# Kernel optimization log

Measured on AMD Instinct MI355X. Metric: run time of the kernel, lower is better.

The kernel has to match this reference:

```python
import jax, jax.numpy as jnp
import numpy as np

H = 4                 # num_heads
GATE_NORM = 16.0      # gate_logit_normalizer
EPS = 1e-5            # RMSNorm eps


def setup_inputs() -> dict:
    key = jax.random.key(0)
    ks = jax.random.split(key, 12)
    B, T, D = 8, 4096, 1024
    Dk_total, Dv_total, Dlow = D // 2, D, 16

    def w(k, shape, fan_in):
        return jax.random.normal(k, shape, dtype=jnp.float32) * (fan_in ** -0.5)

    return {
        "x": jax.random.normal(ks[0], (B, T, D), dtype=jnp.float32),
        "Wq": w(ks[1], (D, Dk_total), D),
        "Wk": w(ks[2], (D, Dk_total), D),
        "Wv": w(ks[3], (D, Dv_total), D),
        "gk_w1": w(ks[4], (D, Dlow), D),
        "gk_w2": w(ks[5], (Dlow, Dk_total), Dlow),
        "gk_b2": jnp.zeros((Dk_total,), dtype=jnp.float32),
        "Wg": w(ks[6], (D, Dv_total), D),
        "g_norm_w": jnp.ones((Dv_total // H,), dtype=jnp.float32),
        "Wo": w(ks[7], (Dv_total, D), Dv_total),
    }


def _gla_forward(x, Wq, Wk, Wv, gk_w1, gk_w2, gk_b2, Wg, g_norm_w, Wo):
    B, T, D = x.shape
    Dk = Wq.shape[1] // H
    Dv = Wv.shape[1] // H

    q = (x @ Wq).reshape(B, T, H, Dk) * (Dk ** -0.5)
    k = (x @ Wk).reshape(B, T, H, Dk)
    v = (x @ Wv).reshape(B, T, H, Dv)
    # low-rank gate logits -> log-space decay gk (<= 0)
    gk = jax.nn.log_sigmoid((x @ gk_w1) @ gk_w2 + gk_b2) / GATE_NORM
    gk = gk.reshape(B, T, H, Dk)

    # recurrent gated linear attention:
    #   S_t = exp(gk_t)[:, None] * S_{t-1} + k_t^T v_t ;  o_t = q_t @ S_t
    def step(S, qkvg):
        qt, kt, vt, gt = qkvg          # each [B, H, Dk|Dv]
        S = jnp.exp(gt)[..., None] * S + kt[..., None] * vt[..., None, :]
        ot = jnp.einsum("bhk,bhkv->bhv", qt, S)
        return S, ot

    S0 = jnp.zeros((B, H, Dk, Dv), dtype=x.dtype)
    tm = lambda a: jnp.swapaxes(a, 0, 1)  # [B,T,...] -> [T,B,...]
    _, o = jax.lax.scan(step, S0, (tm(q), tm(k), tm(v), tm(gk)))
    o = jnp.swapaxes(o, 0, 1)            # [B, T, H, Dv]

    # output gate: RMSNorm(o) * swish(g), per head
    g = (x @ Wg).reshape(B, T, H, Dv)
    o = o * jax.lax.rsqrt(jnp.mean(o * o, axis=-1, keepdims=True) + EPS) * g_norm_w
    o = o * (g * jax.nn.sigmoid(g))
    return o.reshape(B, T, H * Dv) @ Wo


def reference(x, Wq, Wk, Wv, gk_w1, gk_w2, gk_b2, Wg, g_norm_w, Wo):
    return _gla_forward(x, Wq, Wk, Wv, gk_w1, gk_w2, gk_b2, Wg, g_norm_w, Wo)
```

## Files before the change

kernel.cpp:

```cpp
#include <hip/hip_runtime.h>
#include <hip/hip_bf16.h>
#include <cstdint>
#include <cstddef>

typedef __hip_bfloat16 bf16;
typedef __attribute__((ext_vector_type(8))) short short8;
typedef __attribute__((ext_vector_type(4))) float floatx4;

__device__ __forceinline__ void gload_lds16(const void* g, void* l) {
  __builtin_amdgcn_global_load_lds(
      (__attribute__((address_space(1))) void*)(uintptr_t)g,
      (__attribute__((address_space(3))) void*)l, 16, 0, 0);
}

__device__ __forceinline__ short f2bbits(float f) {
  bf16 h = __float2bfloat16(f);
  return __builtin_bit_cast(short, h);
}
__device__ __forceinline__ float b2f(short s) {
  return __bfloat162float(__builtin_bit_cast(bf16, s));
}

__global__ __launch_bounds__(256) void convert_x(const float* __restrict__ x,
                                                 bf16* __restrict__ xb) {
  size_t i = ((size_t)blockIdx.x * 256 + threadIdx.x) * 8;
  float4 f0 = *(const float4*)(x + i);
  float4 f1 = *(const float4*)(x + i + 4);
  short8 r;
  r[0] = f2bbits(f0.x); r[1] = f2bbits(f0.y); r[2] = f2bbits(f0.z); r[3] = f2bbits(f0.w);
  r[4] = f2bbits(f1.x); r[5] = f2bbits(f1.y); r[6] = f2bbits(f1.z); r[7] = f2bbits(f1.w);
  *(short8*)(xb + i) = r;
}

__global__ __launch_bounds__(256) void transpose_w(const float* __restrict__ src,
                                                   bf16* __restrict__ dst, int cols) {
  __shared__ float tile[32][33];
  int n0 = blockIdx.x * 32, k0 = blockIdx.y * 32;
  int tx = threadIdx.x & 31, ty = threadIdx.x >> 5;
#pragma unroll
  for (int i = 0; i < 32; i += 8) {
    int kk = k0 + ty + i, nn = n0 + tx;
    tile[ty + i][tx] = (nn < cols) ? src[(size_t)kk * cols + nn] : 0.0f;
  }
  __syncthreads();
#pragma unroll
  for (int i = 0; i < 32; i += 8) {
    int nn = n0 + ty + i, kk = k0 + tx;
    if (nn < cols) dst[(size_t)nn * 1024 + kk] = __float2bfloat16(tile[tx][ty + i]);
  }
}

#define BARR __builtin_amdgcn_s_barrier()
#define WAITV(n) asm volatile("s_waitcnt vmcnt(" #n ")" ::: "memory")

#define KC 1024
#define K64c (KC * 64)
#define K128c (KC * 128)
#define K32c (KC * 32)

#define STA(buf, h, tau) do { \
  gload_lds16(pA + (size_t)((h) * K64c + (tau) * 64), \
              &lds[(buf) * 16384 + (h) * 8192 + w * 512]); \
  gload_lds16(pA + (size_t)(K128c + (h) * K64c + (tau) * 64), \
              &lds[(buf) * 16384 + (h) * 8192 + 4096 + w * 512]); \
} while (0)

#define STB(buf, h, tau) do { \
  gload_lds16(pB + (size_t)((h) * K32c + (tau) * 64), \
              &lds[32768 + (buf) * 16384 + (h) * 8192 + w * 512]); \
  gload_lds16(pB + (size_t)(K128c + (h) * K32c + (tau) * 64), \
              &lds[32768 + (buf) * 16384 + (h) * 8192 + 4096 + w * 512]); \
} while (0)

#define LDA(mh, buf) do { \
  _Pragma("unroll") \
  for (int mp = 0; mp < 4; ++mp) { \
    const short* p_ = &lds[(buf) * 16384 + (mh) * 8192 + aRow + mp * 1024]; \
    a[mp][0] = *(const short8*)(p_ + g0); \
    a[mp][1] = *(const short8*)(p_ + g1); \
  } \
} while (0)

#define LDB(nh, buf, d0, d1) do { \
  const short* p_ = &lds[(buf) * 16384 + (nh) * 8192 + bRow]; \
  d0[0] = *(const short8*)(p_ + g0); \
  d0[1] = *(const short8*)(p_ + g1); \
  d1[0] = *(const short8*)(p_ + 1024 + g0); \
  d1[1] = *(const short8*)(p_ + 1024 + g1); \
} while (0)

#define MQ(MB, NB, d0, d1) do { \
  __builtin_amdgcn_s_setprio(1); \
  _Pragma("unroll") \
  for (int mp = 0; mp < 4; ++mp) { \
    acc[(MB) + mp][(NB)] = __builtin_amdgcn_mfma_f32_16x16x32_bf16(a[mp][0], d0[0], acc[(MB) + mp][(NB)], 0, 0, 0); \
    acc[(MB) + mp][(NB)] = __builtin_amdgcn_mfma_f32_16x16x32_bf16(a[mp][1], d0[1], acc[(MB) + mp][(NB)], 0, 0, 0); \
    acc[(MB) + mp][(NB) + 1] = __builtin_amdgcn_mfma_f32_16x16x32_bf16(a[mp][0], d1[0], acc[(MB) + mp][(NB) + 1], 0, 0, 0); \
    acc[(MB) + mp][(NB) + 1] = __builtin_amdgcn_mfma_f32_16x16x32_bf16(a[mp][1], d1[1], acc[(MB) + mp][(NB) + 1], 0, 0, 0); \
  } \
  __builtin_amdgcn_s_setprio(0); \
} while (0)

__global__ __launch_bounds__(512, 2) void gemm256(
    const bf16* __restrict__ A, const bf16* __restrict__ Bt,
    const int nTN, const int mode,
    float* __restrict__ oq, float* __restrict__ okk, bf16* __restrict__ ov,
    bf16* __restrict__ ogg, float* __restrict__ oo) {
  extern __shared__ __align__(16) short lds[];
  const int tid = threadIdx.x;
  const int w = tid >> 6, lane = tid & 63;
  const int wr = w >> 2, wc = w & 3;
  const int l15 = lane & 15, lq = lane >> 4;
  const int e7 = lane & 7, l3 = lane >> 3;
  const int gAp = (lane & 7) ^ l3;

  const int cpx = (int)gridDim.x >> 3;
  const int bid = blockIdx.x;
  const int swz = (bid & 7) * cpx + (bid >> 3);
  const int mt = swz / nTN, nt = swz - mt * nTN;
  const int m0 = mt << 8, n0 = nt << 8;

  const bf16* pA = A + (size_t)(m0 + w * 8 + l3) * KC + gAp * 8;
  const bf16* pB = Bt + (size_t)(n0 + (w >> 2) * 64 + (w & 3) * 8 + l3) * KC + gAp * 8;

  const int g0 = ((lq ^ e7) & 7) * 8;
  const int g1 = (((lq + 4) ^ e7) & 7) * 8;
  const int aRow = (wr * 64 + l15) * 64;
  const int bRow = 32768 + (wc * 32 + l15) * 64;

  floatx4 acc[8][4] = {};
  short8 a[4][2], bb0[2], bb1[2], bb2[2], bb3[2];

  STA(0, 0, 0); STB(0, 0, 0); STB(0, 1, 0); STA(0, 1, 0);
  STA(1, 0, 1); STB(1, 1, 1);
  WAITV(4);
  BARR;

  const int nIter = KC >> 7;
  for (int t = 0; t < nIter; ++t) {
    const bool nl = (t < nIter - 1);
    const int t1 = 2 * t + 1, t2 = 2 * t + 2, t3 = 2 * t + 3;
    LDA(0, 0); LDB(0, 0, bb0, bb1); LDB(1, 0, bb2, bb3);
    STA(1, 1, t1);
    BARR; MQ(0, 0, bb0, bb1); BARR;
    STB(1, 0, t1);
    BARR; MQ(0, 2, bb2, bb3); LDA(1, 0); BARR;
    if (nl) STA(0, 0, t2);
    BARR; MQ(4, 2, bb2, bb3); BARR;
    if (nl) STB(0, 1, t2);
    BARR; MQ(4, 0, bb0, bb1);
    if (nl) { WAITV(4); } else { WAITV(0); }
    BARR;
    LDA(0, 1); LDB(0, 1, bb0, bb1); LDB(1, 1, bb2, bb3);
    if (nl) STA(0, 1, t2);
    BARR; MQ(0, 0, bb0, bb1); BARR;
    if (nl) STB(0, 0, t2);
    BARR; MQ(0, 2, bb2, bb3); LDA(1, 1); BARR;
    if (nl) STA(1, 0, t3);
    BARR; MQ(4, 2, bb2, bb3); BARR;
    if (nl) STB(1, 1, t3);
    BARR; MQ(4, 0, bb0, bb1);
    if (nl) { WAITV(4); }
    BARR;
  }

  const int rq = lq * 4;
#pragma unroll
  for (int m = 0; m < 8; ++m) {
#pragma unroll
    for (int n = 0; n < 4; ++n) {
      const int col = n0 + wc * 64 + n * 16 + l15;
#pragma unroll
      for (int r = 0; r < 4; ++r) {
        const size_t row = (size_t)(m0 + wr * 128 + m * 16 + rq + r);
        const float val = acc[m][n][r];
        if (mode == 1) {
          oo[row * 1024 + col] = val;
        } else if (col < 512) {
          oq[row * 512 + col] = val * 0.08838834764831845f;
        } else if (col < 1024) {
          okk[row * 512 + (col - 512)] = val;
        } else if (col < 2048) {
          ov[row * 1024 + (col - 1024)] = __float2bfloat16(val);
        } else {
          ogg[row * 1024 + (col - 2048)] = __float2bfloat16(val);
        }
      }
    }
  }
}

__global__ __launch_bounds__(256) void gate_decay2(const float* __restrict__ x,
                                                   const float* __restrict__ w1,
                                                   const float* __restrict__ w2,
                                                   const float* __restrict__ b2,
                                                   float* __restrict__ gkout) {
  __shared__ float sp[256];
  __shared__ float sz[16];
  const int m0 = blockIdx.x * 4, tid = threadIdx.x;
  const int j = tid & 15, dpart = tid >> 4;
  float w1r[64];
#pragma unroll
  for (int e = 0; e < 64; ++e) w1r[e] = w1[(dpart * 64 + e) * 16 + j];
  float w2r[32];
#pragma unroll
  for (int jj = 0; jj < 16; ++jj) {
    w2r[jj] = w2[jj * 512 + tid];
    w2r[16 + jj] = w2[jj * 512 + tid + 256];
  }
  const float b2a = b2[tid], b2b = b2[tid + 256];
  for (int r = 0; r < 4; ++r) {
    const int m = m0 + r;
    const float* xr = x + (size_t)m * 1024 + dpart * 64;
    float acc = 0.f;
#pragma unroll
    for (int e = 0; e < 64; ++e) acc = fmaf(xr[e], w1r[e], acc);
    sp[tid] = acc;
    __syncthreads();
    if (tid < 16) {
      float s = 0.f;
#pragma unroll
      for (int p = 0; p < 16; ++p) s += sp[p * 16 + tid];
      sz[tid] = s;
    }
    __syncthreads();
    float t = b2a;
#pragma unroll
    for (int jj = 0; jj < 16; ++jj) t = fmaf(sz[jj], w2r[jj], t);
    const float ls = fminf(t, 0.f) - log1pf(__expf(-fabsf(t)));
    gkout[(size_t)m * 512 + tid] = ls * 0.0625f;
    float t2 = b2b;
#pragma unroll
    for (int jj = 0; jj < 16; ++jj) t2 = fmaf(sz[jj], w2r[16 + jj], t2);
    const float ls2 = fminf(t2, 0.f) - log1pf(__expf(-fabsf(t2)));
    gkout[(size_t)m * 512 + tid + 256] = ls2 * 0.0625f;
    if (r < 3) __syncthreads();
  }
}

__global__ __launch_bounds__(128) void chunk_prep(
    const float* __restrict__ q, const float* __restrict__ k,
    const float* __restrict__ gk, bf16* __restrict__ qt,
    bf16* __restrict__ kt, float* __restrict__ dtot) {
  const int cid = blockIdx.x;
  const int c = cid & 63, h = (cid >> 6) & 3, b = cid >> 8;
  const int d = threadIdx.x;
  const size_t rowbase = ((size_t)(b * 4096 + c * 64)) * 512 + h * 128 + d;
  const size_t obase = (size_t)cid * 8192 + d;
  float bsum = 0.f;
  for (int i = 0; i < 64; ++i) {
    const size_t src = rowbase + (size_t)i * 512;
    bsum += gk[src];
    qt[obase + (size_t)i * 128] = __float2bfloat16(q[src] * __expf(bsum));
    kt[obase + (size_t)i * 128] = __float2bfloat16(k[src] * __expf(-bsum));
  }
  dtot[cid * 128 + d] = __expf(bsum);
}

__global__ __launch_bounds__(256) void chunk_intra(
    const bf16* __restrict__ qt, const bf16* __restrict__ kt,
    const float* __restrict__ dtot, const bf16* __restrict__ v,
    bf16* __restrict__ oi, bf16* __restrict__ ut) {
  __shared__ __align__(16) short lA[64 * 72];
  __shared__ __align__(16) short stg[27648];
  short* sQ = stg;
  short* sK = stg + 8704;
  short* sVT = stg;
  short* sKhT = stg + 18432;
  const int cid = blockIdx.x;
  const int c = cid & 63, h = (cid >> 6) & 3, b = cid >> 8;
  const int tid = threadIdx.x, wv = tid >> 6, lane = tid & 63;
  const int l15 = lane & 15, q8 = (lane >> 4) * 8, rq = (lane >> 4) * 4;

  {
    const int row = tid >> 2, seg = (tid & 3) * 32;
    const size_t src = (size_t)cid * 8192 + row * 128 + seg;
    const short8* qs = (const short8*)(qt + src);
    const short8* ks = (const short8*)(kt + src);
    short8* qd = (short8*)&sQ[row * 136 + seg];
    short8* kd = (short8*)&sK[row * 136 + seg];
#pragma unroll
    for (int t = 0; t < 4; ++t) { qd[t] = qs[t]; kd[t] = ks[t]; }
  }
  __syncthreads();
  {
    short8 af[4];
#pragma unroll
    for (int kf = 0; kf < 4; ++kf)
      af[kf] = *(const short8*)&sQ[(wv * 16 + l15) * 136 + kf * 32 + q8];
#pragma unroll
    for (int nt = 0; nt < 4; ++nt) {
      floatx4 accA = {0.f, 0.f, 0.f, 0.f};
#pragma unroll
      for (int kf = 0; kf < 4; ++kf) {
        short8 bfr = *(const short8*)&sK[(nt * 16 + l15) * 136 + kf * 32 + q8];
        accA = __builtin_amdgcn_mfma_f32_16x16x32_bf16(af[kf], bfr, accA, 0, 0, 0);
      }
#pragma unroll
      for (int r = 0; r < 4; ++r) {
        const int i = wv * 16 + rq + r, jj = nt * 16 + l15;
        lA[i * 72 + jj] = f2bbits(jj <= i ? accA[r] : 0.f);
      }
    }
  }
  __syncthreads();
  {
#pragma unroll
    for (int e = 0; e < 8; ++e) {
      const int idx = tid + e * 256;
      const int jj = idx >> 5, n0 = (idx & 31) * 8;
      short8 vv = *(const short8*)(v + ((size_t)(b * 4096 + c * 64 + jj)) * 1024 + h * 256 + n0);
#pragma unroll
      for (int t = 0; t < 8; ++t) sVT[(n0 + t) * 72 + jj] = vv[t];
    }
#pragma unroll
    for (int e = 0; e < 4; ++e) {
      const int idx = tid + e * 256;
      const int jj = idx >> 4, d0 = (idx & 15) * 8;
      short8 kk = *(const short8*)(kt + (size_t)cid * 8192 + jj * 128 + d0);
#pragma unroll
      for (int t = 0; t < 8; ++t)
        sKhT[(d0 + t) * 72 + jj] = f2bbits(b2f(kk[t]) * dtot[cid * 128 + d0 + t]);
    }
  }
  __syncthreads();
  {
    short8 aA0 = *(const short8*)&lA[(wv * 16 + l15) * 72 + q8];
    short8 aA1 = *(const short8*)&lA[(wv * 16 + l15) * 72 + 32 + q8];
#pragma unroll
    for (int nt = 0; nt < 16; ++nt) {
      short8 b0 = *(const short8*)&sVT[(nt * 16 + l15) * 72 + q8];
      short8 b1 = *(const short8*)&sVT[(nt * 16 + l15) * 72 + 32 + q8];
      floatx4 acc = {0.f, 0.f, 0.f, 0.f};
      acc = __builtin_amdgcn_mfma_f32_16x16x32_bf16(aA0, b0, acc, 0, 0, 0);
      acc = __builtin_amdgcn_mfma_f32_16x16x32_bf16(aA1, b1, acc, 0, 0, 0);
#pragma unroll
      for (int r = 0; r < 4; ++r) {
        const int i = wv * 16 + rq + r;
        oi[(size_t)cid * 16384 + i * 256 + nt * 16 + l15] = __builtin_bit_cast(bf16, f2bbits(acc[r]));
      }
    }
  }
  {
    short8 aV[4][2];
#pragma unroll
    for (int mt = 0; mt < 4; ++mt) {
      aV[mt][0] = *(const short8*)&sVT[(wv * 64 + mt * 16 + l15) * 72 + q8];
      aV[mt][1] = *(const short8*)&sVT[(wv * 64 + mt * 16 + l15) * 72 + 32 + q8];
    }
#pragma unroll
    for (int nt = 0; nt < 8; ++nt) {
      short8 b0 = *(const short8*)&sKhT[(nt * 16 + l15) * 72 + q8];
      short8 b1 = *(const short8*)&sKhT[(nt * 16 + l15) * 72 + 32 + q8];
#pragma unroll
      for (int mt = 0; mt < 4; ++mt) {
        floatx4 acc = {0.f, 0.f, 0.f, 0.f};
        acc = __builtin_amdgcn_mfma_f32_16x16x32_bf16(aV[mt][0], b0, acc, 0, 0, 0);
        acc = __builtin_amdgcn_mfma_f32_16x16x32_bf16(aV[mt][1], b1, acc, 0, 0, 0);
#pragma unroll
        for (int r = 0; r < 4; ++r) {
          const int vr = wv * 64 + mt * 16 + rq + r;
          ut[(size_t)cid * 32768 + vr * 128 + nt * 16 + l15] = __builtin_bit_cast(bf16, f2bbits(acc[r]));
        }
      }
    }
  }
}

__global__ __launch_bounds__(256) void state_prop(
    bf16* __restrict__ su,
    const float* __restrict__ dtot) {
  const int ng = blockIdx.x, h = blockIdx.y, b = blockIdx.z;
  const int tid = threadIdx.x;
  const int nrow = ng * 16 + (tid >> 4), kseg = (tid & 15) * 8;
  const int cid0 = (b * 4 + h) * 64;
  size_t a = (size_t)cid0 * 32768 + (size_t)nrow * 128 + kseg;
  float S[8];
#pragma unroll
  for (int e = 0; e < 8; ++e) S[e] = 0.f;
  short8 u0 = *(const short8*)(su + a);
  for (int c = 0; c < 64; ++c) {
    short8 un0;
    if (c < 63) un0 = *(const short8*)(su + a + 32768);
    const float4 d0 = *(const float4*)(dtot + (cid0 + c) * 128 + kseg);
    const float4 d1 = *(const float4*)(dtot + (cid0 + c) * 128 + kseg + 4);
    short8 s0;
#pragma unroll
    for (int e = 0; e < 8; ++e) s0[e] = f2bbits(S[e]);
    *(short8*)(su + a) = s0;
    const float dd[8] = {d0.x, d0.y, d0.z, d0.w, d1.x, d1.y, d1.z, d1.w};
#pragma unroll
    for (int e = 0; e < 8; ++e) S[e] = fmaf(dd[e], S[e], b2f(u0[e]));
    u0 = un0;
    a += 32768;
  }
}

__global__ __launch_bounds__(256, 2) void o_inter(
    const bf16* __restrict__ qt, const bf16* __restrict__ scb,
    const bf16* __restrict__ oi, bf16* __restrict__ opre) {
  __shared__ __align__(16) short sQ[64 * 136];
  const int cid = blockIdx.x;
  const int c = cid & 63, h = (cid >> 6) & 3, b = cid >> 8;
  const int tid = threadIdx.x, wv = tid >> 6, lane = tid & 63;
  const int l15 = lane & 15, q8 = (lane >> 4) * 8, rq = (lane >> 4) * 4;
  {
    const int row = tid >> 2, seg = (tid & 3) * 32;
    const short8* qs = (const short8*)(qt + (size_t)cid * 8192 + row * 128 + seg);
    short8* qd = (short8*)&sQ[row * 136 + seg];
#pragma unroll
    for (int t = 0; t < 4; ++t) qd[t] = qs[t];
  }
  __syncthreads();
  short8 af[4][4];
#pragma unroll
  for (int i = 0; i < 4; ++i)
#pragma unroll
    for (int kf = 0; kf < 4; ++kf)
      af[i][kf] = *(const short8*)&sQ[(i * 16 + l15) * 136 + kf * 32 + q8];
  floatx4 acc[4][4] = {};
#pragma unroll
  for (int j = 0; j < 4; ++j) {
#pragma unroll
    for (int kf = 0; kf < 4; ++kf) {
      short8 bfr = *(const short8*)(scb + (size_t)cid * 32768 +
                                    (size_t)(wv * 64 + j * 16 + l15) * 128 + kf * 32 + q8);
#pragma unroll
      for (int i = 0; i < 4; ++i)
        acc[i][j] = __builtin_amdgcn_mfma_f32_16x16x32_bf16(af[i][kf], bfr, acc[i][j], 0, 0, 0);
    }
  }
  const size_t rowg0 = (size_t)(b * 4096 + c * 64);
#pragma unroll
  for (int i = 0; i < 4; ++i) {
#pragma unroll
    for (int j = 0; j < 4; ++j) {
      const int col = wv * 64 + j * 16 + l15;
#pragma unroll
      for (int r = 0; r < 4; ++r) {
        const int row = i * 16 + rq + r;
        const float val = acc[i][j][r] +
            __bfloat162float(oi[(size_t)cid * 16384 + row * 256 + col]);
        opre[(rowg0 + row) * 1024 + h * 256 + col] = __float2bfloat16(val);
      }
    }
  }
}

__global__ __launch_bounds__(1024) void norm_gate(
    const bf16* __restrict__ o, const bf16* __restrict__ g,
    const float* __restrict__ gnw, bf16* __restrict__ og) {
  __shared__ float sp[16];
  const int tid = threadIdx.x;
  const size_t idx = (size_t)blockIdx.x * 1024 + tid;
  const float f = __bfloat162float(o[idx]);
  float ss = f * f;
#pragma unroll
  for (int mm = 1; mm <= 32; mm <<= 1) ss += __shfl_xor(ss, mm);
  if ((tid & 63) == 0) sp[tid >> 6] = ss;
  __syncthreads();
  const int h4 = (tid >> 8) * 4;
  const float ms = (sp[h4] + sp[h4 + 1] + sp[h4 + 2] + sp[h4 + 3]) * (1.0f / 256.0f);
  const float scale = rsqrtf(ms + 1e-5f) * gnw[tid & 255];
  const float gv = __bfloat162float(g[idx]);
  const float sw = gv * (1.0f / (1.0f + __expf(-gv)));
  og[idx] = __float2bfloat16(f * scale * sw);
}

extern "C" void kernel_launch(void* const* d_in, const int* in_sizes, int n_in,
                              void* d_out, int out_size, void* d_ws, size_t ws_size,
                              hipStream_t stream) {
  const float* x   = (const float*)d_in[0];
  const float* Wq  = (const float*)d_in[1];
  const float* Wk  = (const float*)d_in[2];
  const float* Wv  = (const float*)d_in[3];
  const float* gw1 = (const float*)d_in[4];
  const float* gw2 = (const float*)d_in[5];
  const float* gb2 = (const float*)d_in[6];
  const float* Wg  = (const float*)d_in[7];
  const float* gnw = (const float*)d_in[8];
  const float* Wo  = (const float*)d_in[9];
  float* out = (float*)d_out;

  static bool attr_set = false;
  if (!attr_set) {
    hipFuncSetAttribute(reinterpret_cast<const void*>(gemm256),
                        hipFuncAttributeMaxDynamicSharedMemorySize, 131072);
    attr_set = true;
  }

  const size_t Mi = 1048576;
  uint8_t* w = (uint8_t*)d_ws;
  bf16*  wallT = (bf16*)(w);
  bf16*  woT   = (bf16*)(w + 6 * Mi);
  float* dtot  = (float*)(w + 8 * Mi);
  bf16*  xb    = (bf16*)(w + 9 * Mi);
  bf16*  qt    = (bf16*)(w + 9 * Mi);
  bf16*  ktb   = (bf16*)(w + 41 * Mi);
  bf16*  ogat  = (bf16*)(w + 9 * Mi);
  float* qb    = (float*)(w + 73 * Mi);
  float* kb    = (float*)(w + 137 * Mi);
  bf16*  utb   = (bf16*)(w + 73 * Mi);
  float* gkb   = (float*)(w + 201 * Mi);
  bf16*  oib   = (bf16*)(w + 201 * Mi);
  bf16*  vb    = (bf16*)(w + 265 * Mi);
  bf16*  opre  = (bf16*)(w + 265 * Mi);
  bf16*  gb    = (bf16*)(w + 329 * Mi);

  convert_x<<<dim3(16384), 256, 0, stream>>>(x, xb);
  transpose_w<<<dim3(16, 32), 256, 0, stream>>>(Wq, wallT, 512);
  transpose_w<<<dim3(16, 32), 256, 0, stream>>>(Wk, wallT + (size_t)512 * 1024, 512);
  transpose_w<<<dim3(32, 32), 256, 0, stream>>>(Wv, wallT + (size_t)1024 * 1024, 1024);
  transpose_w<<<dim3(32, 32), 256, 0, stream>>>(Wg, wallT + (size_t)2048 * 1024, 1024);
  transpose_w<<<dim3(32, 32), 256, 0, stream>>>(Wo, woT, 1024);
  gemm256<<<dim3(1536), 512, 131072, stream>>>(xb, wallT, 12, 0, qb, kb, vb, gb, nullptr);
  gate_decay2<<<dim3(8192), 256, 0, stream>>>(x, gw1, gw2, gb2, gkb);
  chunk_prep<<<dim3(2048), 128, 0, stream>>>(qb, kb, gkb, qt, ktb, dtot);
  chunk_intra<<<dim3(2048), 256, 0, stream>>>(qt, ktb, dtot, vb, oib, utb);
  state_prop<<<dim3(16, 4, 8), 256, 0, stream>>>(utb, dtot);
  o_inter<<<dim3(2048), 256, 0, stream>>>(qt, utb, oib, opre);
  norm_gate<<<dim3(32768), 1024, 0, stream>>>(opre, gb, gnw, ogat);
  gemm256<<<dim3(512), 512, 131072, stream>>>(ogat, woT, 4, 1, nullptr, nullptr, nullptr, nullptr, out);
}
```

Before: 1.097 ms.

## Restructure GEMM main loop with double-buffered A registers and fewer barriers

Rewrites the bf16 MFMA GEMM main loop so each iteration covers one 64-wide K step over a fixed 16-step trip count. A-fragment registers are double-buffered (aA/aB) and the next step's LDS fragments are prefetched at the end of each iteration. Most of the paired barriers around each MFMA group are removed, letting global-to-LDS stores overlap with compute. In exchange it raises register pressure, hardcodes K=1024, and relies on the reduced barrier set still preventing LDS read/write races.

```diff
diff --git a/kernel.cpp b/kernel.cpp
--- a/kernel.cpp
+++ b/kernel.cpp
@@ -72,12 +72,12 @@
               &lds[32768 + (buf) * 16384 + (h) * 8192 + 4096 + w * 512]); \
 } while (0)
 
-#define LDA(mh, buf) do { \
+#define LDA2(mh, buf, AR) do { \
   _Pragma("unroll") \
   for (int mp = 0; mp < 4; ++mp) { \
     const short* p_ = &lds[(buf) * 16384 + (mh) * 8192 + aRow + mp * 1024]; \
-    a[mp][0] = *(const short8*)(p_ + g0); \
-    a[mp][1] = *(const short8*)(p_ + g1); \
+    AR[mp][0] = *(const short8*)(p_ + g0); \
+    AR[mp][1] = *(const short8*)(p_ + g1); \
   } \
 } while (0)
 
@@ -89,14 +89,14 @@
   d1[1] = *(const short8*)(p_ + 1024 + g1); \
 } while (0)
 
-#define MQ(MB, NB, d0, d1) do { \
+#define MQ(MB, NB, AR, d0, d1) do { \
   __builtin_amdgcn_s_setprio(1); \
   _Pragma("unroll") \
   for (int mp = 0; mp < 4; ++mp) { \
-    acc[(MB) + mp][(NB)] = __builtin_amdgcn_mfma_f32_16x16x32_bf16(a[mp][0], d0[0], acc[(MB) + mp][(NB)], 0, 0, 0); \
-    acc[(MB) + mp][(NB)] = __builtin_amdgcn_mfma_f32_16x16x32_bf16(a[mp][1], d0[1], acc[(MB) + mp][(NB)], 0, 0, 0); \
-    acc[(MB) + mp][(NB) + 1] = __builtin_amdgcn_mfma_f32_16x16x32_bf16(a[mp][0], d1[0], acc[(MB) + mp][(NB) + 1], 0, 0, 0); \
-    acc[(MB) + mp][(NB) + 1] = __builtin_amdgcn_mfma_f32_16x16x32_bf16(a[mp][1], d1[1], acc[(MB) + mp][(NB) + 1], 0, 0, 0); \
+    acc[(MB) + mp][(NB)] = __builtin_amdgcn_mfma_f32_16x16x32_bf16(AR[mp][0], d0[0], acc[(MB) + mp][(NB)], 0, 0, 0); \
+    acc[(MB) + mp][(NB)] = __builtin_amdgcn_mfma_f32_16x16x32_bf16(AR[mp][1], d0[1], acc[(MB) + mp][(NB)], 0, 0, 0); \
+    acc[(MB) + mp][(NB) + 1] = __builtin_amdgcn_mfma_f32_16x16x32_bf16(AR[mp][0], d1[0], acc[(MB) + mp][(NB) + 1], 0, 0, 0); \
+    acc[(MB) + mp][(NB) + 1] = __builtin_amdgcn_mfma_f32_16x16x32_bf16(AR[mp][1], d1[1], acc[(MB) + mp][(NB) + 1], 0, 0, 0); \
   } \
   __builtin_amdgcn_s_setprio(0); \
 } while (0)
@@ -129,39 +129,35 @@
   const int bRow = 32768 + (wc * 32 + l15) * 64;
 
   floatx4 acc[8][4] = {};
-  short8 a[4][2], bb0[2], bb1[2], bb2[2], bb3[2];
-
-  STA(0, 0, 0); STB(0, 0, 0); STB(0, 1, 0); STA(0, 1, 0);
+  short8 aA[4][2], aB[4][2], p0a[2], p0b[2], p1a[2], p1b[2];
+
+  STA(0, 0, 0); STA(0, 1, 0); STB(0, 0, 0); STB(0, 1, 0);
   STA(1, 0, 1); STB(1, 1, 1);
   WAITV(4);
   BARR;
-
-  const int nIter = KC >> 7;
-  for (int t = 0; t < nIter; ++t) {
-    const bool nl = (t < nIter - 1);
-    const int t1 = 2 * t + 1, t2 = 2 * t + 2, t3 = 2 * t + 3;
-    LDA(0, 0); LDB(0, 0, bb0, bb1); LDB(1, 0, bb2, bb3);
-    STA(1, 1, t1);
-    BARR; MQ(0, 0, bb0, bb1); BARR;
-    STB(1, 0, t1);
-    BARR; MQ(0, 2, bb2, bb3); LDA(1, 0); BARR;
-    if (nl) STA(0, 0, t2);
-    BARR; MQ(4, 2, bb2, bb3); BARR;
-    if (nl) STB(0, 1, t2);
-    BARR; MQ(4, 0, bb0, bb1);
-    if (nl) { WAITV(4); } else { WAITV(0); }
+  LDA2(0, 0, aA); LDB(0, 0, p0a, p0b); LDB(1, 0, p1a, p1b);
+
+#pragma unroll 2
+  for (int t = 0; t < 16; ++t) {
+    const int c = t & 1;
+    if (t < 15) STA(c ^ 1, 1, t + 1);
+    MQ(0, 0, aA, p0a, p0b);
     BARR;
-    LDA(0, 1); LDB(0, 1, bb0, bb1); LDB(1, 1, bb2, bb3);
-    if (nl) STA(0, 1, t2);
-    BARR; MQ(0, 0, bb0, bb1); BARR;
-    if (nl) STB(0, 0, t2);
-    BARR; MQ(0, 2, bb2, bb3); LDA(1, 1); BARR;
-    if (nl) STA(1, 0, t3);
-    BARR; MQ(4, 2, bb2, bb3); BARR;
-    if (nl) STB(1, 1, t3);
-    BARR; MQ(4, 0, bb0, bb1);
-    if (nl) { WAITV(4); }
+    LDA2(1, c, aB);
+    if (t < 15) STB(c ^ 1, 0, t + 1);
+    MQ(0, 2, aA, p1a, p1b);
     BARR;
+    if (t < 14) STA(c, 0, t + 2);
+    MQ(4, 2, aB, p1a, p1b);
+    BARR;
+    if (t < 14) STB(c, 1, t + 2);
+    MQ(4, 0, aB, p0a, p0b);
+    if (t < 14) { WAITV(4); }
+    else if (t == 14) { WAITV(0); }
+    if (t < 15) {
+      BARR;
+      LDA2(0, c ^ 1, aA); LDB(0, c ^ 1, p0a, p0b); LDB(1, c ^ 1, p1a, p1b);
+    }
   }
 
   const int rq = lq * 4;
```

Result: slower. 1.156 ms (+5.5%).

## Fuse RMSNorm-gate into o_inter, store q/k as bf16, stagger GEMM LDS loads

Applied to the files above, without the earlier changes.

Merges the separate norm_gate kernel into the inter-chunk output kernel, computing per-row RMS via shuffles and shared memory so the pre-norm output no longer round-trips through global memory. The QKVG GEMM now writes q and k in bf16 instead of fp32, halving that traffic at some precision cost. GEMM fragment loads from LDS are spread between MFMA groups to lower register pressure. K becomes a runtime parameter.

```diff
diff --git a/kernel.cpp b/kernel.cpp
--- a/kernel.cpp
+++ b/kernel.cpp
@@ -53,22 +53,17 @@
 #define BARR __builtin_amdgcn_s_barrier()
 #define WAITV(n) asm volatile("s_waitcnt vmcnt(" #n ")" ::: "memory")
 
-#define KC 1024
-#define K64c (KC * 64)
-#define K128c (KC * 128)
-#define K32c (KC * 32)
-
 #define STA(buf, h, tau) do { \
-  gload_lds16(pA + (size_t)((h) * K64c + (tau) * 64), \
+  gload_lds16(pA + (size_t)(h) * K64 + (size_t)(tau) * 64, \
               &lds[(buf) * 16384 + (h) * 8192 + w * 512]); \
-  gload_lds16(pA + (size_t)(K128c + (h) * K64c + (tau) * 64), \
+  gload_lds16(pA + K128 + (size_t)(h) * K64 + (size_t)(tau) * 64, \
               &lds[(buf) * 16384 + (h) * 8192 + 4096 + w * 512]); \
 } while (0)
 
 #define STB(buf, h, tau) do { \
-  gload_lds16(pB + (size_t)((h) * K32c + (tau) * 64), \
+  gload_lds16(pB + (size_t)(h) * K32 + (size_t)(tau) * 64, \
               &lds[32768 + (buf) * 16384 + (h) * 8192 + w * 512]); \
-  gload_lds16(pB + (size_t)(K128c + (h) * K32c + (tau) * 64), \
+  gload_lds16(pB + K128 + (size_t)(h) * K32 + (size_t)(tau) * 64, \
               &lds[32768 + (buf) * 16384 + (h) * 8192 + 4096 + w * 512]); \
 } while (0)
 
@@ -102,9 +97,9 @@
 } while (0)
 
 __global__ __launch_bounds__(512, 2) void gemm256(
-    const bf16* __restrict__ A, const bf16* __restrict__ Bt,
+    const bf16* __restrict__ A, const bf16* __restrict__ Bt, const int K,
     const int nTN, const int mode,
-    float* __restrict__ oq, float* __restrict__ okk, bf16* __restrict__ ov,
+    bf16* __restrict__ oq, bf16* __restrict__ okk, bf16* __restrict__ ov,
     bf16* __restrict__ ogg, float* __restrict__ oo) {
   extern __shared__ __align__(16) short lds[];
   const int tid = threadIdx.x;
@@ -120,8 +115,9 @@
   const int mt = swz / nTN, nt = swz - mt * nTN;
   const int m0 = mt << 8, n0 = nt << 8;
 
-  const bf16* pA = A + (size_t)(m0 + w * 8 + l3) * KC + gAp * 8;
-  const bf16* pB = Bt + (size_t)(n0 + (w >> 2) * 64 + (w & 3) * 8 + l3) * KC + gAp * 8;
+  const size_t K64 = (size_t)K * 64, K128 = (size_t)K * 128, K32 = (size_t)K * 32;
+  const bf16* pA = A + (size_t)(m0 + w * 8 + l3) * K + gAp * 8;
+  const bf16* pB = Bt + (size_t)(n0 + (w >> 2) * 64 + (w & 3) * 8 + l3) * K + gAp * 8;
 
   const int g0 = ((lq ^ e7) & 7) * 8;
   const int g1 = (((lq + 4) ^ e7) & 7) * 8;
@@ -136,28 +132,34 @@
   WAITV(4);
   BARR;
 
-  const int nIter = KC >> 7;
+  const int nIter = K >> 7;
   for (int t = 0; t < nIter; ++t) {
     const bool nl = (t < nIter - 1);
     const int t1 = 2 * t + 1, t2 = 2 * t + 2, t3 = 2 * t + 3;
-    LDA(0, 0); LDB(0, 0, bb0, bb1); LDB(1, 0, bb2, bb3);
+    LDA(0, 0); LDB(0, 0, bb0, bb1);
     STA(1, 1, t1);
     BARR; MQ(0, 0, bb0, bb1); BARR;
+    LDB(1, 0, bb2, bb3);
     STB(1, 0, t1);
-    BARR; MQ(0, 2, bb2, bb3); LDA(1, 0); BARR;
+    BARR; MQ(0, 2, bb2, bb3); BARR;
+    LDA(1, 0);
     if (nl) STA(0, 0, t2);
     BARR; MQ(4, 2, bb2, bb3); BARR;
+    LDB(0, 0, bb0, bb1);
     if (nl) STB(0, 1, t2);
     BARR; MQ(4, 0, bb0, bb1);
     if (nl) { WAITV(4); } else { WAITV(0); }
     BARR;
-    LDA(0, 1); LDB(0, 1, bb0, bb1); LDB(1, 1, bb2, bb3);
+    LDA(0, 1); LDB(0, 1, bb0, bb1);
     if (nl) STA(0, 1, t2);
     BARR; MQ(0, 0, bb0, bb1); BARR;
+    LDB(1, 1, bb2, bb3);
     if (nl) STB(0, 0, t2);
-    BARR; MQ(0, 2, bb2, bb3); LDA(1, 1); BARR;
+    BARR; MQ(0, 2, bb2, bb3); BARR;
+    LDA(1, 1);
     if (nl) STA(1, 0, t3);
     BARR; MQ(4, 2, bb2, bb3); BARR;
+    LDB(0, 1, bb0, bb1);
     if (nl) STB(1, 1, t3);
     BARR; MQ(4, 0, bb0, bb1);
     if (nl) { WAITV(4); }
@@ -177,9 +179,9 @@
         if (mode == 1) {
           oo[row * 1024 + col] = val;
         } else if (col < 512) {
-          oq[row * 512 + col] = val * 0.08838834764831845f;
+          oq[row * 512 + col] = __float2bfloat16(val * 0.08838834764831845f);
         } else if (col < 1024) {
-          okk[row * 512 + (col - 512)] = val;
+          okk[row * 512 + (col - 512)] = __float2bfloat16(val);
         } else if (col < 2048) {
           ov[row * 1024 + (col - 1024)] = __float2bfloat16(val);
         } else {
@@ -239,7 +241,7 @@
 }
 
 __global__ __launch_bounds__(128) void chunk_prep(
-    const float* __restrict__ q, const float* __restrict__ k,
+    const bf16* __restrict__ q, const bf16* __restrict__ k,
     const float* __restrict__ gk, bf16* __restrict__ qt,
     bf16* __restrict__ kt, float* __restrict__ dtot) {
   const int cid = blockIdx.x;
@@ -251,8 +253,8 @@
   for (int i = 0; i < 64; ++i) {
     const size_t src = rowbase + (size_t)i * 512;
     bsum += gk[src];
-    qt[obase + (size_t)i * 128] = __float2bfloat16(q[src] * __expf(bsum));
-    kt[obase + (size_t)i * 128] = __float2bfloat16(k[src] * __expf(-bsum));
+    qt[obase + (size_t)i * 128] = __float2bfloat16(__bfloat162float(q[src]) * __expf(bsum));
+    kt[obase + (size_t)i * 128] = __float2bfloat16(__bfloat162float(k[src]) * __expf(-bsum));
   }
   dtot[cid * 128 + d] = __expf(bsum);
 }
@@ -396,10 +398,12 @@
   }
 }
 
-__global__ __launch_bounds__(256, 2) void o_inter(
+__global__ __launch_bounds__(256, 2) void o_inter_norm(
     const bf16* __restrict__ qt, const bf16* __restrict__ scb,
-    const bf16* __restrict__ oi, bf16* __restrict__ opre) {
+    const bf16* __restrict__ oi, const bf16* __restrict__ g,
+    const float* __restrict__ gnw, bf16* __restrict__ og) {
   __shared__ __align__(16) short sQ[64 * 136];
+  __shared__ float sp[64 * 4];
   const int cid = blockIdx.x;
   const int c = cid & 63, h = (cid >> 6) & 3, b = cid >> 8;
   const int tid = threadIdx.x, wv = tid >> 6, lane = tid & 63;
@@ -430,41 +434,45 @@
         acc[i][j] = __builtin_amdgcn_mfma_f32_16x16x32_bf16(af[i][kf], bfr, acc[i][j], 0, 0, 0);
     }
   }
+#pragma unroll
+  for (int i = 0; i < 4; ++i) {
+#pragma unroll
+    for (int r = 0; r < 4; ++r) {
+      const int row = i * 16 + rq + r;
+      float p = 0.f;
+#pragma unroll
+      for (int j = 0; j < 4; ++j) {
+        const int col = wv * 64 + j * 16 + l15;
+        const float v = acc[i][j][r] +
+            __bfloat162float(oi[(size_t)cid * 16384 + row * 256 + col]);
+        acc[i][j][r] = v;
+        p = fmaf(v, v, p);
+      }
+      p += __shfl_xor(p, 1); p += __shfl_xor(p, 2);
+      p += __shfl_xor(p, 4); p += __shfl_xor(p, 8);
+      if (l15 == 0) sp[row * 4 + wv] = p;
+    }
+  }
+  __syncthreads();
   const size_t rowg0 = (size_t)(b * 4096 + c * 64);
 #pragma unroll
   for (int i = 0; i < 4; ++i) {
 #pragma unroll
-    for (int j = 0; j < 4; ++j) {
-      const int col = wv * 64 + j * 16 + l15;
-#pragma unroll
-      for (int r = 0; r < 4; ++r) {
-        const int row = i * 16 + rq + r;
-        const float val = acc[i][j][r] +
-            __bfloat162float(oi[(size_t)cid * 16384 + row * 256 + col]);
-        opre[(rowg0 + row) * 1024 + h * 256 + col] = __float2bfloat16(val);
-      }
-    }
-  }
-}
-
-__global__ __launch_bounds__(1024) void norm_gate(
-    const bf16* __restrict__ o, const bf16* __restrict__ g,
-    const float* __restrict__ gnw, bf16* __restrict__ og) {
-  __shared__ float sp[16];
-  const int tid = threadIdx.x;
-  const size_t idx = (size_t)blockIdx.x * 1024 + tid;
-  const float f = __bfloat162float(o[idx]);
-  float ss = f * f;
-#pragma unroll
-  for (int mm = 1; mm <= 32; mm <<= 1) ss += __shfl_xor(ss, mm);
-  if ((tid & 63) == 0) sp[tid >> 6] = ss;
-  __syncthreads();
-  const int h4 = (tid >> 8) * 4;
-  const float ms = (sp[h4] + sp[h4 + 1] + sp[h4 + 2] + sp[h4 + 3]) * (1.0f / 256.0f);
-  const float scale = rsqrtf(ms + 1e-5f) * gnw[tid & 255];
-  const float gv = __bfloat162float(g[idx]);
-  const float sw = gv * (1.0f / (1.0f + __expf(-gv)));
-  og[idx] = __float2bfloat16(f * scale * sw);
+    for (int r = 0; r < 4; ++r) {
+      const int row = i * 16 + rq + r;
+      const float ms = (sp[row * 4] + sp[row * 4 + 1] + sp[row * 4 + 2] + sp[row * 4 + 3]) *
+                       (1.0f / 256.0f);
+      const float sc = rsqrtf(ms + 1e-5f);
+#pragma unroll
+      for (int j = 0; j < 4; ++j) {
+        const int col = wv * 64 + j * 16 + l15;
+        const size_t gi = (rowg0 + row) * 1024 + h * 256 + col;
+        const float gv = __bfloat162float(g[gi]);
+        const float sw = gv * (1.0f / (1.0f + __expf(-gv)));
+        og[gi] = __float2bfloat16(acc[i][j][r] * sc * gnw[col] * sw);
+      }
+    }
+  }
 }
 
 extern "C" void kernel_launch(void* const* d_in, const int* in_sizes, int n_in,
@@ -497,15 +505,16 @@
   bf16*  xb    = (bf16*)(w + 9 * Mi);
   bf16*  qt    = (bf16*)(w + 9 * Mi);
   bf16*  ktb   = (bf16*)(w + 41 * Mi);
-  bf16*  ogat  = (bf16*)(w + 9 * Mi);
-  float* qb    = (float*)(w + 73 * Mi);
-  float* kb    = (float*)(w + 137 * Mi);
+  float* qbF   = (float*)(w + 73 * Mi);
+  bf16*  qb    = (bf16*)(w + 73 * Mi);
+  bf16*  kb    = (bf16*)(w + 137 * Mi);
   bf16*  utb   = (bf16*)(w + 73 * Mi);
   float* gkb   = (float*)(w + 201 * Mi);
   bf16*  oib   = (bf16*)(w + 201 * Mi);
   bf16*  vb    = (bf16*)(w + 265 * Mi);
-  bf16*  opre  = (bf16*)(w + 265 * Mi);
+  bf16*  ogat  = (bf16*)(w + 265 * Mi);
   bf16*  gb    = (bf16*)(w + 329 * Mi);
+  (void)qbF;
 
   convert_x<<<dim3(16384), 256, 0, stream>>>(x, xb);
   transpose_w<<<dim3(16, 32), 256, 0, stream>>>(Wq, wallT, 512);
@@ -513,12 +522,11 @@
   transpose_w<<<dim3(32, 32), 256, 0, stream>>>(Wv, wallT + (size_t)1024 * 1024, 1024);
   transpose_w<<<dim3(32, 32), 256, 0, stream>>>(Wg, wallT + (size_t)2048 * 1024, 1024);
   transpose_w<<<dim3(32, 32), 256, 0, stream>>>(Wo, woT, 1024);
-  gemm256<<<dim3(1536), 512, 131072, stream>>>(xb, wallT, 12, 0, qb, kb, vb, gb, nullptr);
+  gemm256<<<dim3(1536), 512, 131072, stream>>>(xb, wallT, 1024, 12, 0, qb, kb, vb, gb, nullptr);
   gate_decay2<<<dim3(8192), 256, 0, stream>>>(x, gw1, gw2, gb2, gkb);
   chunk_prep<<<dim3(2048), 128, 0, stream>>>(qb, kb, gkb, qt, ktb, dtot);
   chunk_intra<<<dim3(2048), 256, 0, stream>>>(qt, ktb, dtot, vb, oib, utb);
   state_prop<<<dim3(16, 4, 8), 256, 0, stream>>>(utb, dtot);
-  o_inter<<<dim3(2048), 256, 0, stream>>>(qt, utb, oib, opre);
-  norm_gate<<<dim3(32768), 1024, 0, stream>>>(opre, gb, gnw, ogat);
-  gemm256<<<dim3(512), 512, 131072, stream>>>(ogat, woT, 4, 1, nullptr, nullptr, nullptr, nullptr, out);
-}
+  o_inter_norm<<<dim3(2048), 256, 0, stream>>>(qt, utb, oib, gb, gnw, ogat);
+  gemm256<<<dim3(512), 512, 131072, stream>>>(ogat, woT, 1024, 4, 1, nullptr, nullptr, nullptr, nullptr, out);
+}
```

Result: faster. 1.015 ms (-7.5%).
